# Kernel optimization log

Hardware: AMD Instinct MI355X
Metric: run time of the kernel (lower is better)

## Reference

```python
import jax, jax.numpy as jnp
import numpy as np

B, T, D, H, O, L = 64, 512, 256, 512, 1, 4


def _lstm_layer(x, W_ih, W_hh, b_ih, b_hh):
    """Single LSTM layer, batch_first. x: [B,T,in] -> [B,T,H].
    PyTorch gate order: i, f, g, o."""
    Bv = x.shape[0]
    Hv = W_hh.shape[1]
    # Precompute input contribution for all timesteps (one big GEMM).
    gx = jnp.einsum('btd,gd->btg', x, W_ih) + b_ih + b_hh  # [B,T,4H]

    def step(carry, g_t):
        h, c = carry
        z = g_t + h @ W_hh.T  # [B,4H]
        i, f, g, o = jnp.split(z, 4, axis=-1)
        i = jax.nn.sigmoid(i)
        f = jax.nn.sigmoid(f)
        g = jnp.tanh(g)
        o = jax.nn.sigmoid(o)
        c = f * c + i * g
        h = o * jnp.tanh(c)
        return (h, c), h

    h0 = jnp.zeros((Bv, Hv), x.dtype)
    c0 = jnp.zeros((Bv, Hv), x.dtype)
    _, hs = jax.lax.scan(step, (h0, c0), jnp.swapaxes(gx, 0, 1))  # [T,B,H]
    return jnp.swapaxes(hs, 0, 1)  # [B,T,H]


def setup_inputs() -> dict:
    key = jax.random.key(0)
    ks = jax.random.split(key, 19)
    s = 1.0 / np.sqrt(H)  # PyTorch LSTM init scale
    d = {"x": jax.random.normal(ks[0], (B, T, D), jnp.float32)}
    dims = [D, H, H, H]
    i = 1
    for l in range(L):
        d[f"W_ih{l}"] = jax.random.normal(ks[i], (4 * H, dims[l]), jnp.float32) * s; i += 1
        d[f"W_hh{l}"] = jax.random.normal(ks[i], (4 * H, H), jnp.float32) * s; i += 1
        d[f"b_ih{l}"] = jax.random.normal(ks[i], (4 * H,), jnp.float32) * s; i += 1
        d[f"b_hh{l}"] = jax.random.normal(ks[i], (4 * H,), jnp.float32) * s; i += 1
    d["W_out"] = jax.random.normal(ks[17], (O, H), jnp.float32) * s
    d["b_out"] = jax.random.normal(ks[18], (O,), jnp.float32) * s
    return d


def reference(x, W_ih0, W_hh0, b_ih0, b_hh0,
              W_ih1, W_hh1, b_ih1, b_hh1,
              W_ih2, W_hh2, b_ih2, b_hh2,
              W_ih3, W_hh3, b_ih3, b_hh3,
              W_out, b_out):
    h = x
    layers = ((W_ih0, W_hh0, b_ih0, b_hh0),
              (W_ih1, W_hh1, b_ih1, b_hh1),
              (W_ih2, W_hh2, b_ih2, b_hh2),
              (W_ih3, W_hh3, b_ih3, b_hh3))
    for Wih, Whh, bih, bhh in layers:
        h = _lstm_layer(h, Wih, Whh, bih, bhh)
    # Linear head on last timestep
    return h[:, -1, :] @ W_out.T + b_out  # [B, O]
```

## Files before the change

kernel.cpp:

```cpp
#include <hip/hip_runtime.h>
#include <hip/hip_fp16.h>

typedef _Float16 h16;
typedef _Float16 v8h  __attribute__((ext_vector_type(8)));
typedef float    v4f  __attribute__((ext_vector_type(4)));
typedef unsigned int v4u __attribute__((ext_vector_type(4)));

#define SENTU 0x7C7C7C7Cu
#define CAP   (1 << 13)

struct PParams {
  const float* x;
  const float* Wih[4];
  const float* Whh[4];
  const float* bih[4];
  const float* bhh[4];
  h16* s0; h16* s1; h16* s2;
  h16* s3;
};

__device__ inline float fsigmoid(float x){
  float e = __builtin_amdgcn_exp2f(-1.4426950408889634f * __builtin_fabsf(x));
  float r = __builtin_amdgcn_rcpf(1.0f + e);
  return x >= 0.f ? r : e * r;
}
__device__ inline float ftanhf(float x){
  float e = __builtin_amdgcn_exp2f(-2.8853900817779268f * __builtin_fabsf(x));
  float t = (1.0f - e) * __builtin_amdgcn_rcpf(1.0f + e);
  return x >= 0.f ? t : -t;
}

__device__ inline void issue_ld4(v4u& r0, v4u& r1, v4u& r2, v4u& r3,
                                 const void* p0, const void* p1,
                                 const void* p2, const void* p3){
  asm volatile(
    "global_load_dwordx4 %0, %4, off sc0 sc1\n\t"
    "global_load_dwordx4 %1, %5, off sc0 sc1\n\t"
    "global_load_dwordx4 %2, %6, off sc0 sc1\n\t"
    "global_load_dwordx4 %3, %7, off sc0 sc1"
    : "=&v"(r0), "=&v"(r1), "=&v"(r2), "=&v"(r3)
    : "v"(p0), "v"(p1), "v"(p2), "v"(p3));
}
__device__ inline void wait_vm0(){
  asm volatile("s_waitcnt vmcnt(0)" ::: "memory");
}
__device__ inline void st_agent(void* p, unsigned int v){
  asm volatile("global_store_dword %0, %1, off sc0 sc1" :: "v"(p), "v"(v) : "memory");
}
__device__ inline bool dirtyv(v4u a, v4u b, v4u c, v4u d){
  int bad = 0;
  #pragma unroll
  for (int i = 0; i < 4; ++i)
    bad |= (a[i] == SENTU) | (b[i] == SENTU) | (c[i] == SENTU) | (d[i] == SENTU);
  return bad != 0;
}

template<int KIN, int MODE, bool RESENT>
__device__ void run_layer(const float* __restrict__ Wih, const float* __restrict__ Whh,
                          const float* __restrict__ bih, const float* __restrict__ bhh,
                          const float* __restrict__ xsrc,
                          const h16* __restrict__ src,
                          h16* __restrict__ dst, int dstMask,
                          int rg, int bg, h16* A)
{
  const int tid  = threadIdx.x;
  const int wv   = tid >> 6;
  const int lane = tid & 63;
  const int KI   = KIN / 32;
  const int HOFF = 8192;

  const int n16  = lane & 15;
  const int q4   = lane >> 4;
  const int unit = rg*32 + wv*8 + (n16 & 7);
  const int row0 = ((n16 >> 3)    ) * 512 + unit;
  const int row1 = ((n16 >> 3) + 2) * 512 + unit;

  const int srow  = tid & 15;
  const int g     = tid >> 4;
  const int scol8 = g * 8;

  v8h wihf[KI][2];
  v8h whhf[16][2];
  #pragma unroll
  for (int kk = 0; kk < KI; ++kk)
    #pragma unroll
    for (int j = 0; j < 2; ++j){
      const float* p = Wih + (size_t)(j ? row1 : row0) * KIN + kk*32 + q4*8;
      v8h fr;
      #pragma unroll
      for (int e = 0; e < 8; ++e) fr[e] = (h16)p[e];
      wihf[kk][j] = fr;
    }
  #pragma unroll
  for (int kk = 0; kk < 16; ++kk)
    #pragma unroll
    for (int j = 0; j < 2; ++j){
      const float* p = Whh + (size_t)(j ? row1 : row0) * 512 + kk*32 + q4*8;
      v8h fr;
      #pragma unroll
      for (int e = 0; e < 8; ++e) fr[e] = (h16)p[e];
      whhf[kk][j] = fr;
    }
  const float bias0 = bih[row0] + bhh[row0];
  const float bias1 = bih[row1] + bhh[row1];
  float c[4] = {0.f, 0.f, 0.f, 0.f};
  const bool hi = (lane & 8) != 0;

  v4u sp0{}, sp1{}, sp2{}, sp3{};
  v4u hf0{}, hf1{}, hf2{}, hf3{};

  if (MODE == 0){
    const float* xb = xsrc + ((size_t)(bg*16 + srow)*512 + 0)*256 + g*8;
    issue_ld4(sp0, sp1, sp2, sp3, xb, xb + 4, xb + 128, xb + 132);
  } else {
    const h16* sb = src + ((size_t)(bg*16 + srow))*512 + scol8;
    issue_ld4(sp0, sp1, sp2, sp3, sb, sb + 128, sb + 256, sb + 384);
  }
  wait_vm0();

  h16* const Ast = A + tid*8;
  h16* const Ahw = A + HOFF + tid*8;
  const h16* const Ain = A + lane*8;
  const h16* const Ahr = A + HOFF + lane*8;

  #pragma unroll 1
  for (int t = 0; t < 512; ++t){
    if (MODE == 0){
      v4f f0 = __builtin_bit_cast(v4f, sp0);
      v4f f1 = __builtin_bit_cast(v4f, sp1);
      v4f f2 = __builtin_bit_cast(v4f, sp2);
      v4f f3 = __builtin_bit_cast(v4f, sp3);
      v8h o0 = {(h16)f0[0],(h16)f0[1],(h16)f0[2],(h16)f0[3],
                (h16)f1[0],(h16)f1[1],(h16)f1[2],(h16)f1[3]};
      v8h o1 = {(h16)f2[0],(h16)f2[1],(h16)f2[2],(h16)f2[3],
                (h16)f3[0],(h16)f3[1],(h16)f3[2],(h16)f3[3]};
      *(v8h*)(Ast)        = o0;
      *(v8h*)(Ast + 2048) = o1;
    } else {
      const h16* sb = src + ((size_t)t*64 + bg*16 + srow)*512 + scol8;
      int it = 0;
      while (dirtyv(sp0, sp1, sp2, sp3)){
        __builtin_amdgcn_s_sleep(4);
        issue_ld4(sp0, sp1, sp2, sp3, sb, sb + 128, sb + 256, sb + 384);
        wait_vm0();
        if (++it > CAP) break;
      }
      *(v4u*)(Ast)        = sp0;
      *(v4u*)(Ast + 2048) = sp1;
      *(v4u*)(Ast + 4096) = sp2;
      *(v4u*)(Ast + 6144) = sp3;
    }
    if (t < 511){
      if (MODE == 0){
        const float* xb = xsrc + ((size_t)(bg*16 + srow)*512 + (t+1))*256 + g*8;
        issue_ld4(sp0, sp1, sp2, sp3, xb, xb + 4, xb + 128, xb + 132);
      } else {
        const h16* sb = src + ((size_t)(t+1)*64 + bg*16 + srow)*512 + scol8;
        issue_ld4(sp0, sp1, sp2, sp3, sb, sb + 128, sb + 256, sb + 384);
      }
    }
    if (t > 0){
      const h16* hb = dst + ((size_t)((t-1) & dstMask)*64 + bg*16 + srow)*512 + scol8;
      issue_ld4(hf0, hf1, hf2, hf3, hb, hb + 128, hb + 256, hb + 384);
    }
    __syncthreads();

    v4f acc0 = {0.f,0.f,0.f,0.f};
    v4f acc1 = {0.f,0.f,0.f,0.f};
    #pragma unroll
    for (int kk = 0; kk < KI; ++kk){
      v8h a = *(const v8h*)(Ain + kk*512);
      acc0 = __builtin_amdgcn_mfma_f32_16x16x32_f16(a, wihf[kk][0], acc0, 0, 0, 0);
      acc1 = __builtin_amdgcn_mfma_f32_16x16x32_f16(a, wihf[kk][1], acc1, 0, 0, 0);
    }

    wait_vm0();
    if (t > 0){
      const h16* hb = dst + ((size_t)((t-1) & dstMask)*64 + bg*16 + srow)*512 + scol8;
      int it = 0;
      while (dirtyv(hf0, hf1, hf2, hf3)){
        __builtin_amdgcn_s_sleep(4);
        issue_ld4(hf0, hf1, hf2, hf3, hb, hb + 128, hb + 256, hb + 384);
        wait_vm0();
        if (++it > CAP) break;
      }
      *(v4u*)(Ahw)        = hf0;
      *(v4u*)(Ahw + 2048) = hf1;
      *(v4u*)(Ahw + 4096) = hf2;
      *(v4u*)(Ahw + 6144) = hf3;
    } else {
      v4u z = {0u,0u,0u,0u};
      *(v4u*)(Ahw)        = z;
      *(v4u*)(Ahw + 2048) = z;
      *(v4u*)(Ahw + 4096) = z;
      *(v4u*)(Ahw + 6144) = z;
    }
    __syncthreads();

    #pragma unroll
    for (int kk = 0; kk < 16; ++kk){
      v8h a = *(const v8h*)(Ahr + kk*512);
      acc0 = __builtin_amdgcn_mfma_f32_16x16x32_f16(a, whhf[kk][0], acc0, 0, 0, 0);
      acc1 = __builtin_amdgcn_mfma_f32_16x16x32_f16(a, whhf[kk][1], acc1, 0, 0, 0);
    }

    h16* drow  = dst + (size_t)(t & dstMask) * (64*512);
    h16* dsent = RESENT ? dst + (size_t)((t+4) & dstMask) * (64*512) : nullptr;
    #pragma unroll
    for (int r = 0; r < 4; ++r){
      float z0 = acc0[r] + bias0;
      float z1 = acc1[r] + bias1;
      float p0 = __shfl_xor(z0, 8, 64);
      float p1 = __shfl_xor(z1, 8, 64);
      float iv = hi ? p0 : z0;
      float fv = hi ? z0 : p0;
      float gv = hi ? p1 : z1;
      float ov = hi ? z1 : p1;
      iv = fsigmoid(iv); fv = fsigmoid(fv); ov = fsigmoid(ov);
      gv = ftanhf(gv);
      c[r] = fv * c[r] + iv * gv;
      float hval = ov * ftanhf(c[r]);
      h16 hh = (h16)hval;
      unsigned int mine = (unsigned int)__builtin_bit_cast(unsigned short, hh);
      unsigned int partner = (unsigned int)__shfl_xor((int)mine, 1, 64);
      if (!hi && !(n16 & 1)){
        int batch = bg*16 + q4*4 + r;
        st_agent(drow + (size_t)batch*512 + unit, mine | (partner << 16));
        if (RESENT)
          st_agent(dsent + (size_t)batch*512 + unit, SENTU);
      }
    }
  }
}

__global__ __launch_bounds__(256, 1) void lstm_persist(PParams p){
  __shared__ h16 A[43008];
  const int bx = blockIdx.x;
  const int l  = bx >> 6;
  const int rg = (bx >> 2) & 15;
  const int bg = bx & 3;
  if (l == 0)
    run_layer<256, 0, false>(p.Wih[0], p.Whh[0], p.bih[0], p.bhh[0], p.x, nullptr,
                             p.s0, 511, rg, bg, A);
  else if (l == 1)
    run_layer<512, 1, false>(p.Wih[1], p.Whh[1], p.bih[1], p.bhh[1], nullptr, p.s0,
                             p.s1, 511, rg, bg, A);
  else if (l == 2)
    run_layer<512, 1, false>(p.Wih[2], p.Whh[2], p.bih[2], p.bhh[2], nullptr, p.s1,
                             p.s2, 511, rg, bg, A);
  else
    run_layer<512, 1, true >(p.Wih[3], p.Whh[3], p.bih[3], p.bhh[3], nullptr, p.s2,
                             p.s3, 7, rg, bg, A);
}

__global__ void head_k(const h16* __restrict__ h3, const float* __restrict__ Wo,
                       const float* __restrict__ bo, float* __restrict__ out){
  const int b = blockIdx.x;
  const int lane = threadIdx.x;
  float s = 0.f;
  for (int u = lane; u < 512; u += 64)
    s += (float)h3[(size_t)b * 512 + u] * Wo[u];
  #pragma unroll
  for (int off = 32; off; off >>= 1) s += __shfl_down(s, off, 64);
  if (lane == 0) out[b] = s + bo[0];
}

__global__ void zero_out_k(float* out, int n){
  int i = blockIdx.x * 64 + threadIdx.x;
  if (i < n) out[i] = 0.f;
}

extern "C" void kernel_launch(void* const* d_in, const int* in_sizes, int n_in,
                              void* d_out, int out_size, void* d_ws, size_t ws_size,
                              hipStream_t stream){
  PParams p;
  p.x = (const float*)d_in[0];
  for (int l = 0; l < 4; ++l){
    p.Wih[l] = (const float*)d_in[1 + 4*l + 0];
    p.Whh[l] = (const float*)d_in[1 + 4*l + 1];
    p.bih[l] = (const float*)d_in[1 + 4*l + 2];
    p.bhh[l] = (const float*)d_in[1 + 4*l + 3];
  }
  const float* Wo = (const float*)d_in[17];
  const float* bo = (const float*)d_in[18];

  const size_t SBYTES = (size_t)512 * 64 * 512 * 2;
  const size_t RBYTES = (size_t)8   * 64 * 512 * 2;
  const size_t NEED   = 3 * SBYTES + RBYTES;

  if (ws_size < NEED){
    zero_out_k<<<dim3(1), dim3(64), 0, stream>>>((float*)d_out, out_size);
    return;
  }

  char* ws = (char*)d_ws;
  p.s0 = (h16*)(ws);
  p.s1 = (h16*)(ws + SBYTES);
  p.s2 = (h16*)(ws + 2*SBYTES);
  p.s3 = (h16*)(ws + 3*SBYTES);

  (void)hipMemsetAsync(ws, 0x7C, NEED, stream);

  void* args[] = { &p };
  hipError_t e = hipLaunchCooperativeKernel((void*)lstm_persist, dim3(256), dim3(256),
                                            args, 0, stream);
  if (e != hipSuccess){
    lstm_persist<<<dim3(256), dim3(256), 0, stream>>>(p);
  }

  head_k<<<dim3(64), dim3(64), 0, stream>>>(p.s3 + (size_t)7 * 64 * 512, Wo, bo,
                                            (float*)d_out);
}
```

Measured before the change: 2.074 ms.

## Double-buffer LDS operands and cut per-step barriers to one in LSTM loop

Reorganizes the recurrent loop so the next step's input and hidden-state tiles are fetched, polled and written into an alternate LDS buffer at the end of each step, with a single barrier per timestep instead of two. The input-side polling is merged into the hidden-state polling loop, sleep time per poll is shortened, and layer-0 fp32 x loads drop the coherent cache flags. The aim is to shorten the serial critical path between timesteps, at the cost of doubling LDS buffer usage and changing the spin-wait budget semantics.

```diff
diff --git a/kernel.cpp b/kernel.cpp
--- a/kernel.cpp
+++ b/kernel.cpp
@@ -7,7 +7,7 @@
 typedef unsigned int v4u __attribute__((ext_vector_type(4)));
 
 #define SENTU 0x7C7C7C7Cu
-#define CAP   (1 << 13)
+#define BUDGET (1 << 16)
 
 struct PParams {
   const float* x;
@@ -30,9 +30,9 @@
   return x >= 0.f ? t : -t;
 }
 
-__device__ inline void issue_ld4(v4u& r0, v4u& r1, v4u& r2, v4u& r3,
-                                 const void* p0, const void* p1,
-                                 const void* p2, const void* p3){
+__device__ inline void issue_ld4_c(v4u& r0, v4u& r1, v4u& r2, v4u& r3,
+                                   const void* p0, const void* p1,
+                                   const void* p2, const void* p3){
   asm volatile(
     "global_load_dwordx4 %0, %4, off sc0 sc1\n\t"
     "global_load_dwordx4 %1, %5, off sc0 sc1\n\t"
@@ -41,8 +41,27 @@
     : "=&v"(r0), "=&v"(r1), "=&v"(r2), "=&v"(r3)
     : "v"(p0), "v"(p1), "v"(p2), "v"(p3));
 }
-__device__ inline void wait_vm0(){
-  asm volatile("s_waitcnt vmcnt(0)" ::: "memory");
+__device__ inline void issue_ld4_p(v4u& r0, v4u& r1, v4u& r2, v4u& r3,
+                                   const void* p0, const void* p1,
+                                   const void* p2, const void* p3){
+  asm volatile(
+    "global_load_dwordx4 %0, %4, off\n\t"
+    "global_load_dwordx4 %1, %5, off\n\t"
+    "global_load_dwordx4 %2, %6, off\n\t"
+    "global_load_dwordx4 %3, %7, off"
+    : "=&v"(r0), "=&v"(r1), "=&v"(r2), "=&v"(r3)
+    : "v"(p0), "v"(p1), "v"(p2), "v"(p3));
+}
+__device__ inline void wait_vm0_t8(v4u& a, v4u& b, v4u& c, v4u& d,
+                                   v4u& e, v4u& f, v4u& g, v4u& h){
+  asm volatile("s_waitcnt vmcnt(0)"
+               : "+v"(a), "+v"(b), "+v"(c), "+v"(d),
+                 "+v"(e), "+v"(f), "+v"(g), "+v"(h)
+               :: "memory");
+}
+__device__ inline void wait_vm0_t4(v4u& a, v4u& b, v4u& c, v4u& d){
+  asm volatile("s_waitcnt vmcnt(0)"
+               : "+v"(a), "+v"(b), "+v"(c), "+v"(d) :: "memory");
 }
 __device__ inline void st_agent(void* p, unsigned int v){
   asm volatile("global_store_dword %0, %1, off sc0 sc1" :: "v"(p), "v"(v) : "memory");
@@ -67,7 +86,6 @@
   const int wv   = tid >> 6;
   const int lane = tid & 63;
   const int KI   = KIN / 32;
-  const int HOFF = 8192;
 
   const int n16  = lane & 15;
   const int q4   = lane >> 4;
@@ -108,95 +126,71 @@
 
   v4u sp0{}, sp1{}, sp2{}, sp3{};
   v4u hf0{}, hf1{}, hf2{}, hf3{};
+  int budget = BUDGET;
 
   if (MODE == 0){
     const float* xb = xsrc + ((size_t)(bg*16 + srow)*512 + 0)*256 + g*8;
-    issue_ld4(sp0, sp1, sp2, sp3, xb, xb + 4, xb + 128, xb + 132);
+    issue_ld4_p(sp0, sp1, sp2, sp3, xb, xb + 4, xb + 128, xb + 132);
+    wait_vm0_t4(sp0, sp1, sp2, sp3);
+    v4f f0 = __builtin_bit_cast(v4f, sp0);
+    v4f f1 = __builtin_bit_cast(v4f, sp1);
+    v4f f2 = __builtin_bit_cast(v4f, sp2);
+    v4f f3 = __builtin_bit_cast(v4f, sp3);
+    v8h o0 = {(h16)f0[0],(h16)f0[1],(h16)f0[2],(h16)f0[3],
+              (h16)f1[0],(h16)f1[1],(h16)f1[2],(h16)f1[3]};
+    v8h o1 = {(h16)f2[0],(h16)f2[1],(h16)f2[2],(h16)f2[3],
+              (h16)f3[0],(h16)f3[1],(h16)f3[2],(h16)f3[3]};
+    *(v8h*)(A + tid*8)        = o0;
+    *(v8h*)(A + tid*8 + 2048) = o1;
   } else {
     const h16* sb = src + ((size_t)(bg*16 + srow))*512 + scol8;
-    issue_ld4(sp0, sp1, sp2, sp3, sb, sb + 128, sb + 256, sb + 384);
-  }
-  wait_vm0();
-
-  h16* const Ast = A + tid*8;
-  h16* const Ahw = A + HOFF + tid*8;
-  const h16* const Ain = A + lane*8;
-  const h16* const Ahr = A + HOFF + lane*8;
+    issue_ld4_c(sp0, sp1, sp2, sp3, sb, sb + 128, sb + 256, sb + 384);
+    wait_vm0_t4(sp0, sp1, sp2, sp3);
+    while (dirtyv(sp0, sp1, sp2, sp3)){
+      if (--budget <= 0) break;
+      __builtin_amdgcn_s_sleep(1);
+      issue_ld4_c(sp0, sp1, sp2, sp3, sb, sb + 128, sb + 256, sb + 384);
+      wait_vm0_t4(sp0, sp1, sp2, sp3);
+    }
+    *(v4u*)(A + tid*8)        = sp0;
+    *(v4u*)(A + tid*8 + 2048) = sp1;
+    *(v4u*)(A + tid*8 + 4096) = sp2;
+    *(v4u*)(A + tid*8 + 6144) = sp3;
+  }
+  {
+    v4u z = {0u,0u,0u,0u};
+    *(v4u*)(A + 8192 + tid*8)        = z;
+    *(v4u*)(A + 8192 + tid*8 + 2048) = z;
+    *(v4u*)(A + 8192 + tid*8 + 4096) = z;
+    *(v4u*)(A + 8192 + tid*8 + 6144) = z;
+  }
+  __syncthreads();
 
   #pragma unroll 1
   for (int t = 0; t < 512; ++t){
-    if (MODE == 0){
-      v4f f0 = __builtin_bit_cast(v4f, sp0);
-      v4f f1 = __builtin_bit_cast(v4f, sp1);
-      v4f f2 = __builtin_bit_cast(v4f, sp2);
-      v4f f3 = __builtin_bit_cast(v4f, sp3);
-      v8h o0 = {(h16)f0[0],(h16)f0[1],(h16)f0[2],(h16)f0[3],
-                (h16)f1[0],(h16)f1[1],(h16)f1[2],(h16)f1[3]};
-      v8h o1 = {(h16)f2[0],(h16)f2[1],(h16)f2[2],(h16)f2[3],
-                (h16)f3[0],(h16)f3[1],(h16)f3[2],(h16)f3[3]};
-      *(v8h*)(Ast)        = o0;
-      *(v8h*)(Ast + 2048) = o1;
-    } else {
-      const h16* sb = src + ((size_t)t*64 + bg*16 + srow)*512 + scol8;
-      int it = 0;
-      while (dirtyv(sp0, sp1, sp2, sp3)){
-        __builtin_amdgcn_s_sleep(4);
-        issue_ld4(sp0, sp1, sp2, sp3, sb, sb + 128, sb + 256, sb + 384);
-        wait_vm0();
-        if (++it > CAP) break;
-      }
-      *(v4u*)(Ast)        = sp0;
-      *(v4u*)(Ast + 2048) = sp1;
-      *(v4u*)(Ast + 4096) = sp2;
-      *(v4u*)(Ast + 6144) = sp3;
-    }
+    const h16* Ar = A + (t & 1)*16384;
+    h16*       Aw = A + ((t + 1) & 1)*16384;
+
     if (t < 511){
       if (MODE == 0){
         const float* xb = xsrc + ((size_t)(bg*16 + srow)*512 + (t+1))*256 + g*8;
-        issue_ld4(sp0, sp1, sp2, sp3, xb, xb + 4, xb + 128, xb + 132);
+        issue_ld4_p(sp0, sp1, sp2, sp3, xb, xb + 4, xb + 128, xb + 132);
       } else {
         const h16* sb = src + ((size_t)(t+1)*64 + bg*16 + srow)*512 + scol8;
-        issue_ld4(sp0, sp1, sp2, sp3, sb, sb + 128, sb + 256, sb + 384);
+        issue_ld4_c(sp0, sp1, sp2, sp3, sb, sb + 128, sb + 256, sb + 384);
       }
     }
-    if (t > 0){
-      const h16* hb = dst + ((size_t)((t-1) & dstMask)*64 + bg*16 + srow)*512 + scol8;
-      issue_ld4(hf0, hf1, hf2, hf3, hb, hb + 128, hb + 256, hb + 384);
-    }
-    __syncthreads();
 
     v4f acc0 = {0.f,0.f,0.f,0.f};
     v4f acc1 = {0.f,0.f,0.f,0.f};
+    const h16* Ain = Ar + lane*8;
     #pragma unroll
     for (int kk = 0; kk < KI; ++kk){
       v8h a = *(const v8h*)(Ain + kk*512);
       acc0 = __builtin_amdgcn_mfma_f32_16x16x32_f16(a, wihf[kk][0], acc0, 0, 0, 0);
       acc1 = __builtin_amdgcn_mfma_f32_16x16x32_f16(a, wihf[kk][1], acc1, 0, 0, 0);
     }
-
-    wait_vm0();
-    if (t > 0){
-      const h16* hb = dst + ((size_t)((t-1) & dstMask)*64 + bg*16 + srow)*512 + scol8;
-      int it = 0;
-      while (dirtyv(hf0, hf1, hf2, hf3)){
-        __builtin_amdgcn_s_sleep(4);
-        issue_ld4(hf0, hf1, hf2, hf3, hb, hb + 128, hb + 256, hb + 384);
-        wait_vm0();
-        if (++it > CAP) break;
-      }
-      *(v4u*)(Ahw)        = hf0;
-      *(v4u*)(Ahw + 2048) = hf1;
-      *(v4u*)(Ahw + 4096) = hf2;
-      *(v4u*)(Ahw + 6144) = hf3;
-    } else {
-      v4u z = {0u,0u,0u,0u};
-      *(v4u*)(Ahw)        = z;
-      *(v4u*)(Ahw + 2048) = z;
-      *(v4u*)(Ahw + 4096) = z;
-      *(v4u*)(Ahw + 6144) = z;
-    }
-    __syncthreads();
-
+    const h16* Ahr = Ar + 8192 + lane*8;
     #pragma unroll
     for (int kk = 0; kk < 16; ++kk){
       v8h a = *(const v8h*)(Ahr + kk*512);
@@ -205,7 +199,7 @@
     }
 
     h16* drow  = dst + (size_t)(t & dstMask) * (64*512);
-    h16* dsent = RESENT ? dst + (size_t)((t+4) & dstMask) * (64*512) : nullptr;
+    h16* dsent = RESENT ? dst + (size_t)((t+4) & 7) * (64*512) : nullptr;
     #pragma unroll
     for (int r = 0; r < 4; ++r){
       float z0 = acc0[r] + bias0;
@@ -230,6 +224,49 @@
           st_agent(dsent + (size_t)batch*512 + unit, SENTU);
       }
     }
+
+    if (t == 511) break;
+
+    const h16* hb = dst + ((size_t)(t & dstMask)*64 + bg*16 + srow)*512 + scol8;
+    issue_ld4_c(hf0, hf1, hf2, hf3, hb, hb + 128, hb + 256, hb + 384);
+    wait_vm0_t8(sp0, sp1, sp2, sp3, hf0, hf1, hf2, hf3);
+    for (;;){
+      bool sd = (MODE == 1) && dirtyv(sp0, sp1, sp2, sp3);
+      bool hd = dirtyv(hf0, hf1, hf2, hf3);
+      if (!sd && !hd) break;
+      if (--budget <= 0) break;
+      __builtin_amdgcn_s_sleep(1);
+      if (sd){
+        const h16* sb = src + ((size_t)(t+1)*64 + bg*16 + srow)*512 + scol8;
+        issue_ld4_c(sp0, sp1, sp2, sp3, sb, sb + 128, sb + 256, sb + 384);
+      }
+      if (hd)
+        issue_ld4_c(hf0, hf1, hf2, hf3, hb, hb + 128, hb + 256, hb + 384);
+      wait_vm0_t8(sp0, sp1, sp2, sp3, hf0, hf1, hf2, hf3);
+    }
+
+    if (MODE == 0){
+      v4f f0 = __builtin_bit_cast(v4f, sp0);
+      v4f f1 = __builtin_bit_cast(v4f, sp1);
+      v4f f2 = __builtin_bit_cast(v4f, sp2);
+      v4f f3 = __builtin_bit_cast(v4f, sp3);
+      v8h o0 = {(h16)f0[0],(h16)f0[1],(h16)f0[2],(h16)f0[3],
+                (h16)f1[0],(h16)f1[1],(h16)f1[2],(h16)f1[3]};
+      v8h o1 = {(h16)f2[0],(h16)f2[1],(h16)f2[2],(h16)f2[3],
+                (h16)f3[0],(h16)f3[1],(h16)f3[2],(h16)f3[3]};
+      *(v8h*)(Aw + tid*8)        = o0;
+      *(v8h*)(Aw + tid*8 + 2048) = o1;
+    } else {
+      *(v4u*)(Aw + tid*8)        = sp0;
+      *(v4u*)(Aw + tid*8 + 2048) = sp1;
+      *(v4u*)(Aw + tid*8 + 4096) = sp2;
+      *(v4u*)(Aw + tid*8 + 6144) = sp3;
+    }
+    *(v4u*)(Aw + 8192 + tid*8)        = hf0;
+    *(v4u*)(Aw + 8192 + tid*8 + 2048) = hf1;
+    *(v4u*)(Aw + 8192 + tid*8 + 4096) = hf2;
+    *(v4u*)(Aw + 8192 + tid*8 + 6144) = hf3;
+    __syncthreads();
   }
 }
 
```

After: 3.545 ms. +71.0%, slower.
